# Kernel tuning notes

Hardware: AMD Instinct MI355X
Metric: run time of the kernel (lower is better)

## Reference

```python
import jax, jax.numpy as jnp
import numpy as np

COST_CLASS, COST_BBOX, COST_GIOU = 1.0, 5.0, 2.0


def box_cxcywh_to_xyxy(b):
    cx, cy, w, h = jnp.split(b, 4, axis=-1)
    return jnp.concatenate([cx - 0.5 * w, cy - 0.5 * h, cx + 0.5 * w, cy + 0.5 * h], axis=-1)


def generalized_box_iou(a, b):
    # a: [N,4], b: [T,4] in xyxy -> [N,T]
    area_a = (a[:, 2] - a[:, 0]) * (a[:, 3] - a[:, 1])
    area_b = (b[:, 2] - b[:, 0]) * (b[:, 3] - b[:, 1])
    lt = jnp.maximum(a[:, None, :2], b[None, :, :2])
    rb = jnp.minimum(a[:, None, 2:], b[None, :, 2:])
    wh = jnp.clip(rb - lt, 0.0)
    inter = wh[..., 0] * wh[..., 1]
    union = area_a[:, None] + area_b[None, :] - inter
    iou = inter / union
    lt_e = jnp.minimum(a[:, None, :2], b[None, :, :2])
    rb_e = jnp.maximum(a[:, None, 2:], b[None, :, 2:])
    wh_e = jnp.clip(rb_e - lt_e, 0.0)
    area_e = wh_e[..., 0] * wh_e[..., 1]
    return iou - (area_e - union) / area_e


def cost_matrix(pred_logits, pred_boxes, tgt_labels, tgt_boxes):
    B, Q, _ = pred_logits.shape
    probs = jax.nn.softmax(pred_logits.reshape(B * Q, -1), axis=-1)
    pb = pred_boxes.reshape(B * Q, 4)
    tl = tgt_labels.reshape(-1)
    tb = tgt_boxes.reshape(-1, 4)
    cc = -probs[:, tl]                                              # [BQ, BM]
    cb = jnp.sum(jnp.abs(pb[:, None, :] - tb[None, :, :]), axis=-1)  # L1 cdist
    cg = -generalized_box_iou(box_cxcywh_to_xyxy(pb), box_cxcywh_to_xyxy(tb))
    C = COST_CLASS * cc + COST_BBOX * cb + COST_GIOU * cg
    return C.reshape(B, Q, -1)


def hungarian(cost):
    # Jonker-Volgenant shortest-augmenting-path assignment.
    # cost: [n, m] with n <= m; returns the column assigned to each row, [n] int32.
    n, m = cost.shape
    INF = jnp.float32(1e30)

    def solve_row(i, uvp):
        u, v, p = uvp  # u:[n+1] row potentials (+dummy), v:[m+1], p:[m+1] row assigned per col
        p = p.at[m].set(i)  # virtual start column m holds the new row
        state = (jnp.int32(m), u, v, p,
                 jnp.full(m + 1, INF, jnp.float32),   # minv
                 jnp.zeros(m + 1, bool),              # used
                 jnp.zeros(m + 1, jnp.int32))         # way

        def cond(s):
            j0, _, _, p, _, _, _ = s
            return p[j0] != -1

        def body(s):
            j0, u, v, p, minv, used, way = s
            used = used.at[j0].set(True)
            i0 = p[j0]
            cur = jnp.where(used[:m], INF, cost[i0] - u[i0] - v[:m])
            better = cur < minv[:m]
            minv = minv.at[:m].set(jnp.where(better, cur, minv[:m]))
            way = way.at[:m].set(jnp.where(better, j0, way[:m]))
            masked = jnp.where(used[:m], INF, minv[:m])
            j1 = jnp.argmin(masked).astype(jnp.int32)
            delta = masked[j1]
            u = u.at[jnp.where(used, p, n)].add(jnp.where(used, delta, 0.0))
            v = jnp.where(used, v - delta, v)
            minv = jnp.where(used, minv, minv - delta)
            return (j1, u, v, p, minv, used, way)

        j0, u, v, p, minv, used, way = jax.lax.while_loop(cond, body, state)

        def a_cond(s):
            return s[0] != m

        def a_body(s):
            j0, p = s
            j1 = way[j0]
            return (j1, p.at[j0].set(p[j1]))

        _, p = jax.lax.while_loop(a_cond, a_body, (j0, p))
        return (u, v, p)

    u0 = jnp.zeros(n + 1, jnp.float32)
    v0 = jnp.zeros(m + 1, jnp.float32)
    p0 = jnp.full(m + 1, -1, jnp.int32)
    _, _, p = jax.lax.fori_loop(0, n, solve_row, (u0, v0, p0))
    row_of_col = p[:m]
    cols = jnp.arange(m, dtype=jnp.int32)
    col_of_row = jnp.zeros(n + 1, jnp.int32).at[
        jnp.where(row_of_col >= 0, row_of_col, n)].set(cols)
    return col_of_row[:n]


def setup_inputs() -> dict:
    key = jax.random.key(0)
    k1, k2, k3, k4 = jax.random.split(key, 4)
    B, Q, NCLS, M = 32, 300, 92, 50
    return {
        'pred_logits': jax.random.normal(k1, (B, Q, NCLS), jnp.float32),
        'pred_boxes': jax.random.uniform(k2, (B, Q, 4), dtype=jnp.float32),
        'tgt_labels': jax.random.randint(k3, (B, M), 0, NCLS),
        'tgt_boxes': jax.random.uniform(k4, (B, M, 4), dtype=jnp.float32),
    }


def reference(pred_logits, pred_boxes, tgt_labels, tgt_boxes):
    B, Q, _ = pred_logits.shape
    M = tgt_labels.shape[1]
    C = cost_matrix(pred_logits, pred_boxes, tgt_labels, tgt_boxes)  # [B, Q, B*M]
    # per-image block of columns: C[i, :, i*M:(i+1)*M]
    C4 = C.reshape(B, Q, B, M)
    C_per = jnp.transpose(jnp.diagonal(C4, axis1=0, axis2=2), (2, 0, 1))  # [B, Q, M]
    q = jax.vmap(hungarian)(jnp.transpose(C_per, (0, 2, 1)))  # [B, M]: query per target
    order = jnp.argsort(q, axis=1).astype(jnp.int32)
    pred_idx = jnp.take_along_axis(q, order, axis=1)  # sorted query indices
    gt_idx = order                                     # matching target indices
    return pred_idx, gt_idx, C
```

## Files before the change

kernel.cpp:

```cpp
#include <hip/hip_runtime.h>
#include <hip/hip_bf16.h>

#define NB   32
#define NQ   300
#define NCLS 92
#define NM   50
#define BM   (NB * NM)
#define BQ   (NB * NQ)
#define HM   NQ
#define HN   NM
#define PITCH 305
#define BIG  1e30f
#define HUNG_BLOCKS NB
#define COST_ROWS_PER_BLOCK 16
#define COST_BLOCKS (BQ / COST_ROWS_PER_BLOCK)
#define NBLOCKS (HUNG_BLOCKS + COST_BLOCKS)

typedef float vf4 __attribute__((ext_vector_type(4)));

#define FENCE() __threadfence_block()

__device__ __forceinline__ float wred_max(float v) {
#pragma unroll
  for (int m = 1; m < 64; m <<= 1) v = fmaxf(v, __shfl_xor(v, m, 64));
  return v;
}
__device__ __forceinline__ float wred_sum(float v) {
#pragma unroll
  for (int m = 1; m < 64; m <<= 1) v += __shfl_xor(v, m, 64);
  return v;
}
__device__ __forceinline__ float wred_min(float v) {
#pragma unroll
  for (int m = 1; m < 64; m <<= 1) v = fminf(v, __shfl_xor(v, m, 64));
  return v;
}

__device__ __forceinline__ float pair_cost(float ax1, float ay1, float ax2,
                                           float ay2, float areaA,
                                           const float4& pb, const float4& t,
                                           float negprob) {
  float cb = fabsf(pb.x - t.x) + fabsf(pb.y - t.y) +
             fabsf(pb.z - t.z) + fabsf(pb.w - t.w);
  float bx1 = t.x - 0.5f * t.z, by1 = t.y - 0.5f * t.w;
  float bx2 = t.x + 0.5f * t.z, by2 = t.y + 0.5f * t.w;
  float areaB = (bx2 - bx1) * (by2 - by1);
  float iw = fmaxf(fminf(ax2, bx2) - fmaxf(ax1, bx1), 0.f);
  float ih = fmaxf(fminf(ay2, by2) - fmaxf(ay1, by1), 0.f);
  float inter = iw * ih;
  float uni = areaA + areaB - inter;
  float iou = inter / uni;
  float ew = fmaxf(fmaxf(ax2, bx2) - fminf(ax1, bx1), 0.f);
  float eh = fmaxf(fmaxf(ay2, by2) - fminf(ay1, by1), 0.f);
  float areaE = ew * eh;
  float giou = iou - (areaE - uni) / areaE;
  return (negprob + 5.f * cb) - 2.f * giou;
}

__device__ __forceinline__ void wave_softmax(const float* __restrict__ lrow,
                                             float* prow, int lane) {
  float x0 = (lane < NCLS) ? lrow[lane] : -BIG;
  float x1 = (lane + 64 < NCLS) ? lrow[lane + 64] : -BIG;
  float mx = wred_max(fmaxf(x0, x1));
  float e0 = expf(x0 - mx), e1 = expf(x1 - mx);
  float s = wred_sum(e0 + e1);
  if (lane < NCLS) prow[lane] = e0 / s;
  if (lane + 64 < NCLS) prow[lane + 64] = e1 / s;
  FENCE();
}

__global__ __launch_bounds__(1024) void fused_kernel(
    const float* __restrict__ logits, const float* __restrict__ pboxes,
    const int* __restrict__ tlab, const float* __restrict__ tbox,
    float* __restrict__ outp) {
  __shared__ float hc[HN * PITCH];
  __shared__ float probs_s[16][NCLS];
  __shared__ int   p[HM + 1];
  __shared__ int   way[HM];
  __shared__ int   qarr[HN];

  float* C = outp + 2 * BM;
  int tid = threadIdx.x, wave = tid >> 6, lane = tid & 63;

  if (blockIdx.x >= HUNG_BLOCKS) {
    int row = (blockIdx.x - HUNG_BLOCKS) * COST_ROWS_PER_BLOCK + wave;
    wave_softmax(logits + (size_t)row * NCLS, probs_s[wave], lane);

    float4 pb = reinterpret_cast<const float4*>(pboxes)[row];
    float ax1 = pb.x - 0.5f * pb.z, ay1 = pb.y - 0.5f * pb.w;
    float ax2 = pb.x + 0.5f * pb.z, ay2 = pb.y + 0.5f * pb.w;
    float areaA = (ax2 - ax1) * (ay2 - ay1);

    const float4* tbv = reinterpret_cast<const float4*>(tbox);
    const int4*   tlv = reinterpret_cast<const int4*>(tlab);
    vf4* crow = reinterpret_cast<vf4*>(C + (size_t)row * BM);
    for (int q4 = lane; q4 < BM / 4; q4 += 64) {
      int4 cls = tlv[q4];
      int clsa[4] = {cls.x, cls.y, cls.z, cls.w};
      vf4 o;
#pragma unroll
      for (int e = 0; e < 4; e++) {
        float4 t = tbv[q4 * 4 + e];
        o[e] = pair_cost(ax1, ay1, ax2, ay2, areaA, pb, t,
                         -probs_s[wave][clsa[e]]);
      }
      __builtin_nontemporal_store(o, &crow[q4]);
    }
    return;
  }

  int b = blockIdx.x;

  for (int x = tid; x <= HM; x += 1024) p[x] = -1;

  float4 t_reg = make_float4(0.f, 0.f, 0.f, 0.f);
  int cls_reg = 0;
  if (lane < NM) {
    t_reg = reinterpret_cast<const float4*>(tbox)[b * NM + lane];
    cls_reg = tlab[b * NM + lane];
  }

  const float4* pbv = reinterpret_cast<const float4*>(pboxes);
  for (int q = wave; q < NQ; q += 16) {
    wave_softmax(logits + (size_t)(b * NQ + q) * NCLS, probs_s[wave], lane);
    float4 pb = pbv[b * NQ + q];
    float ax1 = pb.x - 0.5f * pb.z, ay1 = pb.y - 0.5f * pb.w;
    float ax2 = pb.x + 0.5f * pb.z, ay2 = pb.y + 0.5f * pb.w;
    float areaA = (ax2 - ax1) * (ay2 - ay1);
    if (lane < NM) {
      float negp = -probs_s[wave][cls_reg];
      hc[lane * PITCH + q] =
          pair_cost(ax1, ay1, ax2, ay2, areaA, pb, t_reg, negp);
    }
  }
  __syncthreads();
  if (wave != 0) return;


  float u_reg = 0.f;
  int am_reg = 0;
  if (lane < HN) {
    float mn = BIG; int amv = 0;
    for (int j = 0; j < HM; j++) {
      float vv = hc[lane * PITCH + j];
      if (vv < mn) { mn = vv; amv = j; }
    }
    u_reg = mn; am_reg = amv;
  }

  unsigned amask = 0;
  unsigned long long pending = 0;
  for (int i = 0; i < HN; i++) {
    int jm = __shfl(am_reg, i, 64);
    unsigned mrem = __shfl(amask, jm & 63, 64);
    if (!((mrem >> (jm >> 6)) & 1u)) {
      if (lane == (jm & 63)) amask |= 1u << (jm >> 6);
      if (lane == 0) p[jm] = i;
    } else {
      pending |= 1ull << i;
    }
  }
  FENCE();

  float v_r[5], minv_r[5];
#pragma unroll
  for (int k = 0; k < 5; k++) v_r[k] = 0.f;

  while (pending) {
    int i_start = (int)__ffsll((long long)pending) - 1;
    pending &= pending - 1;
#pragma unroll
    for (int k = 0; k < 5; k++) minv_r[k] = BIG;
    unsigned usedc = 0;
    unsigned long long used_rows = 1ull << i_start;
    int i0 = i_start, j0 = HM, jfree = -1;
    float ui0 = __shfl(u_reg, i0, 64);

    while (true) {
      float best = BIG; int bj = 0;
#pragma unroll
      for (int k = 0; k < 5; k++) {
        int j = lane + 64 * k;
        if (j < HM && !((usedc >> k) & 1u)) {
          float cur = hc[i0 * PITCH + j] - ui0 - v_r[k];
          if (cur < minv_r[k]) { minv_r[k] = cur; way[j] = j0; }
          if (minv_r[k] < best) { best = minv_r[k]; bj = j; }
        }
      }
      float wmin = wred_min(best);
      unsigned long long ball = __ballot(best == wmin);
      int src = (int)__ffsll((long long)ball) - 1;
      int j1 = __shfl(bj, src, 64);
      float delta = wmin;

      int psel = p[j1];

      if ((used_rows >> lane) & 1ull) u_reg += delta;
#pragma unroll
      for (int k = 0; k < 5; k++) {
        int j = lane + 64 * k;
        if (j < HM) {
          if ((usedc >> k) & 1u) v_r[k] -= delta;
          else                   minv_r[k] -= delta;
        }
      }
      if (lane == (j1 & 63)) usedc |= 1u << (j1 >> 6);

      if (psel == -1) { jfree = j1; break; }
      i0 = psel;
      used_rows |= 1ull << i0;
      ui0 = __shfl(u_reg, i0, 64);
      j0 = j1;
    }

    int jj = jfree;
    while (jj != HM) {
      int jn = way[jj];
      int pv = (jn == HM) ? i_start : p[jn];
      p[jj] = pv;
      jj = jn;
    }
    FENCE();
  }

  for (int j = lane; j < HM; j += 64) {
    int r = p[j];
    if (r >= 0) qarr[r] = j;
  }
  FENCE();
  if (lane < HN) {
    int qi = qarr[lane];
    int rank = 0;
    for (int t = 0; t < HN; t++) rank += (qarr[t] < qi);
    outp[(size_t)b * NM + rank] = (float)qi;
    outp[BM + (size_t)b * NM + rank] = (float)lane;
  }
}

extern "C" void kernel_launch(void* const* d_in, const int* in_sizes, int n_in,
                              void* d_out, int out_size, void* d_ws, size_t ws_size,
                              hipStream_t stream) {
  const float* logits = (const float*)d_in[0];
  const float* pboxes = (const float*)d_in[1];
  const int*   tlab   = (const int*)d_in[2];
  const float* tbox   = (const float*)d_in[3];
  float* out = (float*)d_out;

  fused_kernel<<<dim3(NBLOCKS), dim3(1024), 0, stream>>>(
      logits, pboxes, tlab, tbox, out);
}
```

Before: 125.4 us.

## Use DPP/readlane wave reductions and register-gathered softmax in Hungarian blocks

Replaces shuffle-based wave reductions with DPP row/broadcast ops followed by a readlane, and swaps the uniform-index __shfl calls in the Hungarian loop for readlane. The Hungarian blocks' cost build now gathers the target-class logit with shuffles instead of writing the full softmax row to shared memory and reading it back. The row-min scan uses two independent accumulators with a tie-break that keeps the first index. These changes shorten the serial latency of the single-wave augmenting-path loop, at the cost of relying on wave-uniform indices and a DPP sequence that must reduce all 64 lanes correctly.

Measured after the change: 117.4 us. -6.4%, faster.

```diff
diff --git a/kernel.cpp b/kernel.cpp
--- a/kernel.cpp
+++ b/kernel.cpp
@@ -1,5 +1,4 @@
 #include <hip/hip_runtime.h>
-#include <hip/hip_bf16.h>
 
 #define NB   32
 #define NQ   300
@@ -20,20 +19,60 @@
 
 #define FENCE() __threadfence_block()
 
-__device__ __forceinline__ float wred_max(float v) {
-#pragma unroll
-  for (int m = 1; m < 64; m <<= 1) v = fmaxf(v, __shfl_xor(v, m, 64));
-  return v;
-}
-__device__ __forceinline__ float wred_sum(float v) {
-#pragma unroll
-  for (int m = 1; m < 64; m <<= 1) v += __shfl_xor(v, m, 64);
-  return v;
-}
-__device__ __forceinline__ float wred_min(float v) {
-#pragma unroll
-  for (int m = 1; m < 64; m <<= 1) v = fminf(v, __shfl_xor(v, m, 64));
-  return v;
+#define DPP_XOR1  0xB1
+#define DPP_XOR2  0x4E
+#define DPP_HMIRR 0x141
+#define DPP_MIRR  0x140
+#define DPP_BC15  0x142
+#define DPP_BC31  0x143
+
+template <int C_>
+__device__ __forceinline__ float dppk(float v) {
+  return __int_as_float(__builtin_amdgcn_update_dpp(
+      __float_as_int(v), __float_as_int(v), C_, 0xf, 0xf, false));
+}
+template <int C_>
+__device__ __forceinline__ float dppz(float v) {
+  return __int_as_float(
+      __builtin_amdgcn_update_dpp(0, __float_as_int(v), C_, 0xf, 0xf, true));
+}
+
+__device__ __forceinline__ float rl63(float v) {
+  return __int_as_float(__builtin_amdgcn_readlane(__float_as_int(v), 63));
+}
+__device__ __forceinline__ int rli(int v, int l) {
+  return __builtin_amdgcn_readlane(v, l);
+}
+__device__ __forceinline__ float rlf(float v, int l) {
+  return __int_as_float(__builtin_amdgcn_readlane(__float_as_int(v), l));
+}
+
+__device__ __forceinline__ float wredu_max(float v) {
+  v = fmaxf(v, dppk<DPP_XOR1>(v));
+  v = fmaxf(v, dppk<DPP_XOR2>(v));
+  v = fmaxf(v, dppk<DPP_HMIRR>(v));
+  v = fmaxf(v, dppk<DPP_MIRR>(v));
+  v = fmaxf(v, dppk<DPP_BC15>(v));
+  v = fmaxf(v, dppk<DPP_BC31>(v));
+  return rl63(v);
+}
+__device__ __forceinline__ float wredu_min(float v) {
+  v = fminf(v, dppk<DPP_XOR1>(v));
+  v = fminf(v, dppk<DPP_XOR2>(v));
+  v = fminf(v, dppk<DPP_HMIRR>(v));
+  v = fminf(v, dppk<DPP_MIRR>(v));
+  v = fminf(v, dppk<DPP_BC15>(v));
+  v = fminf(v, dppk<DPP_BC31>(v));
+  return rl63(v);
+}
+__device__ __forceinline__ float wredu_sum(float v) {
+  v += dppz<DPP_XOR1>(v);
+  v += dppz<DPP_XOR2>(v);
+  v += dppz<DPP_HMIRR>(v);
+  v += dppz<DPP_MIRR>(v);
+  v += dppz<DPP_BC15>(v);
+  v += dppz<DPP_BC31>(v);
+  return rl63(v);
 }
 
 __device__ __forceinline__ float pair_cost(float ax1, float ay1, float ax2,
@@ -59,12 +98,12 @@
 
 __device__ __forceinline__ void wave_softmax(const float* __restrict__ lrow,
                                              float* prow, int lane) {
-  float x0 = (lane < NCLS) ? lrow[lane] : -BIG;
+  float x0 = lrow[lane];
   float x1 = (lane + 64 < NCLS) ? lrow[lane + 64] : -BIG;
-  float mx = wred_max(fmaxf(x0, x1));
+  float mx = wredu_max(fmaxf(x0, x1));
   float e0 = expf(x0 - mx), e1 = expf(x1 - mx);
-  float s = wred_sum(e0 + e1);
-  if (lane < NCLS) prow[lane] = e0 / s;
+  float s = wredu_sum(e0 + e1);
+  prow[lane] = e0 / s;
   if (lane + 64 < NCLS) prow[lane + 64] = e1 / s;
   FENCE();
 }
@@ -122,13 +161,22 @@
 
   const float4* pbv = reinterpret_cast<const float4*>(pboxes);
   for (int q = wave; q < NQ; q += 16) {
-    wave_softmax(logits + (size_t)(b * NQ + q) * NCLS, probs_s[wave], lane);
+    const float* lrow = logits + (size_t)(b * NQ + q) * NCLS;
+    float x0 = lrow[lane];
+    float x1 = (lane + 64 < NCLS) ? lrow[lane + 64] : -BIG;
+    float mx = wredu_max(fmaxf(x0, x1));
+    float e0 = expf(x0 - mx), e1 = expf(x1 - mx);
+    float s = wredu_sum(e0 + e1);
+    float g0 = __shfl(x0, cls_reg, 64);
+    float g1 = __shfl(x1, cls_reg, 64);
+    float xsel = (cls_reg < 64) ? g0 : g1;
+    float negp = -(expf(xsel - mx) / s);
+
     float4 pb = pbv[b * NQ + q];
     float ax1 = pb.x - 0.5f * pb.z, ay1 = pb.y - 0.5f * pb.w;
     float ax2 = pb.x + 0.5f * pb.z, ay2 = pb.y + 0.5f * pb.w;
     float areaA = (ax2 - ax1) * (ay2 - ay1);
     if (lane < NM) {
-      float negp = -probs_s[wave][cls_reg];
       hc[lane * PITCH + q] =
           pair_cost(ax1, ay1, ax2, ay2, areaA, pb, t_reg, negp);
     }
@@ -140,19 +188,24 @@
   float u_reg = 0.f;
   int am_reg = 0;
   if (lane < HN) {
-    float mn = BIG; int amv = 0;
-    for (int j = 0; j < HM; j++) {
-      float vv = hc[lane * PITCH + j];
-      if (vv < mn) { mn = vv; amv = j; }
-    }
-    u_reg = mn; am_reg = amv;
+    const float* r = &hc[lane * PITCH];
+    float mn0 = BIG, mn1 = BIG;
+    int a0 = 0, a1 = 1;
+    for (int j = 0; j < HM; j += 2) {
+      float va = r[j], vb = r[j + 1];
+      if (va < mn0) { mn0 = va; a0 = j; }
+      if (vb < mn1) { mn1 = vb; a1 = j + 1; }
+    }
+    bool takeOdd = (mn1 < mn0) || (mn1 == mn0 && a1 < a0);
+    u_reg = takeOdd ? mn1 : mn0;
+    am_reg = takeOdd ? a1 : a0;
   }
 
   unsigned amask = 0;
   unsigned long long pending = 0;
   for (int i = 0; i < HN; i++) {
-    int jm = __shfl(am_reg, i, 64);
-    unsigned mrem = __shfl(amask, jm & 63, 64);
+    int jm = rli(am_reg, i);
+    unsigned mrem = (unsigned)rli((int)amask, jm & 63);
     if (!((mrem >> (jm >> 6)) & 1u)) {
       if (lane == (jm & 63)) amask |= 1u << (jm >> 6);
       if (lane == 0) p[jm] = i;
@@ -174,23 +227,24 @@
     unsigned usedc = 0;
     unsigned long long used_rows = 1ull << i_start;
     int i0 = i_start, j0 = HM, jfree = -1;
-    float ui0 = __shfl(u_reg, i0, 64);
+    float ui0 = rlf(u_reg, i0);
 
     while (true) {
       float best = BIG; int bj = 0;
+      const float* hrow = &hc[i0 * PITCH];
 #pragma unroll
       for (int k = 0; k < 5; k++) {
         int j = lane + 64 * k;
         if (j < HM && !((usedc >> k) & 1u)) {
-          float cur = hc[i0 * PITCH + j] - ui0 - v_r[k];
+          float cur = hrow[j] - ui0 - v_r[k];
           if (cur < minv_r[k]) { minv_r[k] = cur; way[j] = j0; }
           if (minv_r[k] < best) { best = minv_r[k]; bj = j; }
         }
       }
-      float wmin = wred_min(best);
+      float wmin = wredu_min(best);
       unsigned long long ball = __ballot(best == wmin);
       int src = (int)__ffsll((long long)ball) - 1;
-      int j1 = __shfl(bj, src, 64);
+      int j1 = rli(bj, src);
       float delta = wmin;
 
       int psel = p[j1];
@@ -209,7 +263,7 @@
       if (psel == -1) { jfree = j1; break; }
       i0 = psel;
       used_rows |= 1ull << i0;
-      ui0 = __shfl(u_reg, i0, 64);
+      ui0 = rlf(u_reg, i0);
       j0 = j1;
     }
 
```
